# Optimization experiments

Measured on AMD Instinct MI355X. Metric: run time of the kernel, lower is better.

The kernel has to match this reference:

```python
import jax, jax.numpy as jnp
import numpy as np

B, S, H, NH, L, FF, V, T = 16, 256, 768, 12, 12, 3072, 30522, 9
DH = H // NH
LN_EPS = 1e-12


def _ln(x, g, b):
    m = jnp.mean(x, axis=-1, keepdims=True)
    v = jnp.mean((x - m) ** 2, axis=-1, keepdims=True)
    return (x - m) * jax.lax.rsqrt(v + LN_EPS) * g + b


def setup_inputs():
    key = jax.random.key(0)
    ks = jax.random.split(key, 20)
    n = lambda i, shape: jax.random.normal(ks[i], shape, jnp.float32) * 0.02
    lengths = jax.random.randint(ks[0], (B,), S // 2, S + 1)
    attention_mask = (jnp.arange(S)[None, :] < lengths[:, None]).astype(jnp.int32)
    return {
        "input_ids": jax.random.randint(ks[1], (B, S), 0, V),
        "attention_mask": attention_mask,
        "labels": jax.random.randint(ks[2], (B, S), 0, T),
        "word_emb": n(3, (V, H)),
        "pos_emb": n(4, (512, H)),
        "type_emb": n(5, (2, H)),
        "emb_g": jnp.ones((H,), jnp.float32), "emb_b": jnp.zeros((H,), jnp.float32),
        "lWq": n(6, (L, H, H)), "lbq": jnp.zeros((L, H), jnp.float32),
        "lWk": n(7, (L, H, H)), "lbk": jnp.zeros((L, H), jnp.float32),
        "lWv": n(8, (L, H, H)), "lbv": jnp.zeros((L, H), jnp.float32),
        "lWo": n(9, (L, H, H)), "lbo": jnp.zeros((L, H), jnp.float32),
        "lg1": jnp.ones((L, H), jnp.float32), "lb1": jnp.zeros((L, H), jnp.float32),
        "lWi": n(10, (L, H, FF)), "lbi": jnp.zeros((L, FF), jnp.float32),
        "lWf": n(11, (L, FF, H)), "lbf": jnp.zeros((L, H), jnp.float32),
        "lg2": jnp.ones((L, H), jnp.float32), "lb2": jnp.zeros((L, H), jnp.float32),
        "cls_W": n(12, (H, T)), "cls_b": jnp.zeros((T,), jnp.float32),
        "crf_start": jax.random.uniform(ks[13], (T,), jnp.float32, -0.1, 0.1),
        "crf_end": jax.random.uniform(ks[14], (T,), jnp.float32, -0.1, 0.1),
        "crf_trans": jax.random.uniform(ks[15], (T, T), jnp.float32, -0.1, 0.1),
    }


def _encoder(input_ids, attention_mask, word_emb, pos_emb, type_emb, emb_g, emb_b, layer_stack, cls_W, cls_b):
    x = word_emb[input_ids] + pos_emb[:S][None] + type_emb[0][None, None]  # [B,S,H]
    x = _ln(x, emb_g, emb_b)
    bias = (1.0 - attention_mask.astype(jnp.float32))[:, None, None, :] * -1e9  # [B,1,1,S]
    scale = 1.0 / np.sqrt(DH).astype(np.float32)

    def layer(h, p):
        Wq, bq, Wk, bk, Wv, bv, Wo, bo, g1, b1, Wi, bi, Wf, bf, g2, b2 = p
        q = (h @ Wq + bq).reshape(B, S, NH, DH)
        k = (h @ Wk + bk).reshape(B, S, NH, DH)
        v = (h @ Wv + bv).reshape(B, S, NH, DH)
        att = jax.nn.softmax(jnp.einsum('bqhd,bkhd->bhqk', q, k) * scale + bias, axis=-1)
        ctx = jnp.einsum('bhqk,bkhd->bqhd', att, v).reshape(B, S, H)
        h = _ln(h + ctx @ Wo + bo, g1, b1)
        ff = jax.nn.gelu(h @ Wi + bi, approximate=False) @ Wf + bf
        h = _ln(h + ff, g2, b2)
        return h, None

    x, _ = jax.lax.scan(layer, x, layer_stack)
    return x @ cls_W + cls_b  # [B,S,T]


def _crf_llh(em, tg, m, start, end, trans):
    # pytorch-crf forward, reduction='sum'. em [B,Lc,T], tg [B,Lc] int, m [B,Lc] bool
    mf = m.astype(em.dtype)
    em_sc = jnp.take_along_axis(em, tg[..., None], axis=-1)[..., 0]  # [B,Lc]
    tr_sc = trans[tg[:, :-1], tg[:, 1:]]                             # [B,Lc-1]
    num = start[tg[:, 0]] + em_sc[:, 0] + jnp.sum(mf[:, 1:] * (tr_sc + em_sc[:, 1:]), axis=1)
    seq_ends = jnp.sum(m.astype(jnp.int32), axis=1) - 1
    last_tag = jnp.take_along_axis(tg, seq_ends[:, None], axis=1)[:, 0]
    num = num + end[last_tag]

    def step(score, xs):
        em_t, m_t = xs
        nxt = jax.nn.logsumexp(score[:, :, None] + trans[None] + em_t[:, None, :], axis=1)
        return jnp.where(m_t[:, None], nxt, score), None

    score0 = start[None] + em[:, 0]
    score, _ = jax.lax.scan(step, score0, (em[:, 1:].transpose(1, 0, 2), m[:, 1:].transpose(1, 0)))
    den = jax.nn.logsumexp(score + end[None], axis=1)
    return jnp.sum(num - den)


def _viterbi(em, start, end, trans):
    # decode over the FULL sequence with all-ones mask (matches crf.decode(logits))
    def step(score, em_t):
        cand = score[:, :, None] + trans[None] + em_t[:, None, :]  # [B,T,T]
        return jnp.max(cand, axis=1), jnp.argmax(cand, axis=1)

    score0 = start[None] + em[:, 0]
    score, hist = jax.lax.scan(step, score0, em[:, 1:].transpose(1, 0, 2))  # hist [S-1,B,T]
    last = jnp.argmax(score + end[None], axis=1)  # [B]

    def back(tag, h):
        prev = jnp.take_along_axis(h, tag[:, None], axis=1)[:, 0]
        return prev, prev

    _, rev = jax.lax.scan(back, last, hist, reverse=True)  # rev[i] = tag at time i, i in [0,S-2]
    tags = jnp.concatenate([rev.transpose(1, 0), last[:, None]], axis=1)  # [B,S]
    return tags.astype(jnp.float32)


def reference(input_ids, attention_mask, labels, word_emb, pos_emb, type_emb, emb_g, emb_b,
              lWq, lbq, lWk, lbk, lWv, lbv, lWo, lbo, lg1, lb1, lWi, lbi, lWf, lbf, lg2, lb2,
              cls_W, cls_b, crf_start, crf_end, crf_trans):
    layer_stack = (lWq, lbq, lWk, lbk, lWv, lbv, lWo, lbo, lg1, lb1, lWi, lbi, lWf, lbf, lg2, lb2)
    logits = _encoder(input_ids, attention_mask, word_emb, pos_emb, type_emb, emb_g, emb_b, layer_stack, cls_W, cls_b)
    str_lens = jnp.sum(attention_mask, axis=-1)
    pos = jnp.arange(S)[None, :]
    mask = attention_mask.astype(bool) & (pos > 0) & (pos != (str_lens - 1)[:, None])
    tags_in = jnp.where(mask, labels, jnp.zeros_like(labels))
    loss = -_crf_llh(logits[:, 1:], tags_in[:, 1:], mask[:, 1:], crf_start, crf_end, crf_trans)
    tags = _viterbi(logits, crf_start, crf_end, crf_trans)
    return (loss, tags)
```

## Files before the change

kernel.cpp:

```cpp
#include <hip/hip_runtime.h>

#define B_ 16
#define S_ 256
#define H_ 768
#define NH_ 12
#define DH_ 64
#define L_ 12
#define FF_ 3072
#define T_ 9
#define NTOK (B_*S_)

#define AS1 __attribute__((address_space(1)))
#define AS3 __attribute__((address_space(3)))

typedef __attribute__((ext_vector_type(8))) short bfrag;
typedef __attribute__((ext_vector_type(8))) unsigned short us8;
typedef __attribute__((ext_vector_type(4))) float f4;

#define LOG2E_ 1.4426950408889634f
#define LN2_   0.6931471805599453f

__device__ inline unsigned short f2bf(float x) {
    unsigned u = __builtin_bit_cast(unsigned, x);
    return (unsigned short)((u + 0x7fffu + ((u >> 16) & 1u)) >> 16);
}
__device__ inline float bf2f(unsigned short h) {
    unsigned u = ((unsigned)h) << 16;
    return __builtin_bit_cast(float, u);
}
__device__ inline void pack8(const float* v, us8& h, us8& l) {
    #pragma unroll
    for (int j = 0; j < 8; j++) {
        unsigned short hh = f2bf(v[j]);
        h[j] = hh;
        l[j] = f2bf(v[j] - bf2f(hh));
    }
}

__global__ __launch_bounds__(256) void k_conv_w(
    const float* __restrict__ Wq, const float* __restrict__ Wk,
    const float* __restrict__ Wv, const float* __restrict__ Wo,
    const float* __restrict__ Wi, const float* __restrict__ Wf,
    const float* __restrict__ bq, const float* __restrict__ bk, const float* __restrict__ bv,
    float* __restrict__ qkvbias, unsigned short* __restrict__ Wpk)
{
    int bid = blockIdx.x;
    int tid = threadIdx.x;
    if (bid == 0) {
        for (int i = tid; i < 3 * H_; i += 256)
            qkvbias[i] = (i < H_) ? bq[i] : (i < 2 * H_) ? bk[i - H_] : bv[i - 2 * H_];
    }
    const float* src; int Kd, Nd; size_t doff; int t;
    if (bid < 576)       { int m = bid / 144; src = (m == 0) ? Wq : (m == 1) ? Wk : (m == 2) ? Wv : Wo;
                           Kd = H_; Nd = H_; doff = (size_t)m * 73728; t = bid % 144; }
    else if (bid < 1152) { src = Wi; Kd = H_; Nd = FF_; doff = 294912; t = bid - 576; }
    else                 { src = Wf; Kd = FF_; Nd = H_; doff = 589824; t = bid - 1152; }
    int ntn = Nd / 64;
    int tk = t / ntn, tn = t % ntn;
    int k0 = tk * 64, n0 = tn * 64;
    __shared__ float tile[64][65];
    int r = tid >> 6, c = tid & 63;
    #pragma unroll
    for (int i = 0; i < 16; i++)
        tile[r + i * 4][c] = src[(size_t)(k0 + r + i * 4) * Nd + n0 + c];
    __syncthreads();
    #pragma unroll
    for (int e = 0; e < 2; e++) {
        int item = tid * 2 + e;
        int nl = item >> 3, kb = item & 7;
        float v8[8];
        #pragma unroll
        for (int j = 0; j < 8; j++) v8[j] = tile[kb * 8 + j][nl];
        us8 h, l; pack8(v8, h, l);
        unsigned short* p = Wpk + (doff + (size_t)(n0 + nl) * (Kd / 8) + (k0 / 8 + kb)) * 16;
        *reinterpret_cast<us8*>(p) = h;
        *reinterpret_cast<us8*>(p + 8) = l;
    }
}

__global__ __launch_bounds__(128) void k_embed_ln(
    const int* __restrict__ ids, const float* __restrict__ wemb,
    const float* __restrict__ pemb, const float* __restrict__ temb,
    const float* __restrict__ g, const float* __restrict__ bb,
    float* __restrict__ out, unsigned short* __restrict__ out_pk)
{
    int tok = blockIdx.x;
    int s = tok & (S_ - 1);
    int id = ids[tok];
    int tid = threadIdx.x;
    bool act = tid < 96;
    int idx = tid * 8;
    float v8[8];
    float sum = 0.f;
    if (act) {
        const float4* w4 = reinterpret_cast<const float4*>(wemb + (size_t)id * H_ + idx);
        const float4* p4 = reinterpret_cast<const float4*>(pemb + (size_t)s * H_ + idx);
        const float4* t4 = reinterpret_cast<const float4*>(temb + idx);
        #pragma unroll
        for (int q = 0; q < 2; q++) {
            float4 a = w4[q], b = p4[q], c = t4[q];
            v8[q*4+0] = a.x + b.x + c.x; v8[q*4+1] = a.y + b.y + c.y;
            v8[q*4+2] = a.z + b.z + c.z; v8[q*4+3] = a.w + b.w + c.w;
        }
        #pragma unroll
        for (int j = 0; j < 8; j++) sum += v8[j];
    }
    __shared__ float wsum[2], wvar[2];
    #pragma unroll
    for (int o = 32; o > 0; o >>= 1) sum += __shfl_xor(sum, o);
    if ((tid & 63) == 0) wsum[tid >> 6] = sum;
    __syncthreads();
    float mean = (wsum[0] + wsum[1]) * (1.0f / H_);
    float vs = 0.f;
    if (act) {
        for (int j = 0; j < 8; j++) { float d = v8[j] - mean; vs += d * d; }
    }
    #pragma unroll
    for (int o = 32; o > 0; o >>= 1) vs += __shfl_xor(vs, o);
    if ((tid & 63) == 0) wvar[tid >> 6] = vs;
    __syncthreads();
    float inv = 1.0f / sqrtf((wvar[0] + wvar[1]) * (1.0f / H_) + 1e-12f);
    if (act) {
        float o8[8];
        #pragma unroll
        for (int j = 0; j < 8; j++) o8[j] = (v8[j] - mean) * inv * g[idx + j] + bb[idx + j];
        float4* d4 = reinterpret_cast<float4*>(out + (size_t)tok * H_ + idx);
        d4[0] = make_float4(o8[0], o8[1], o8[2], o8[3]);
        d4[1] = make_float4(o8[4], o8[5], o8[6], o8[7]);
        us8 h, l; pack8(o8, h, l);
        unsigned short* p = out_pk + ((size_t)tok * 96 + tid) * 16;
        *reinterpret_cast<us8*>(p) = h;
        *reinterpret_cast<us8*>(p + 8) = l;
    }
}

__global__ __launch_bounds__(128) void k_res_ln(
    const float* __restrict__ x, const float* __restrict__ res,
    const float* __restrict__ g, const float* __restrict__ bb,
    float* __restrict__ out, unsigned short* __restrict__ out_pk)
{
    int tok = blockIdx.x;
    int tid = threadIdx.x;
    bool act = tid < 96;
    int idx = tid * 8;
    float v8[8];
    float sum = 0.f;
    if (act) {
        const float4* x4 = reinterpret_cast<const float4*>(x + (size_t)tok * H_ + idx);
        const float4* r4 = reinterpret_cast<const float4*>(res + (size_t)tok * H_ + idx);
        #pragma unroll
        for (int q = 0; q < 2; q++) {
            float4 a = x4[q], b = r4[q];
            v8[q*4+0] = a.x + b.x; v8[q*4+1] = a.y + b.y;
            v8[q*4+2] = a.z + b.z; v8[q*4+3] = a.w + b.w;
        }
        #pragma unroll
        for (int j = 0; j < 8; j++) sum += v8[j];
    }
    __shared__ float wsum[2], wvar[2];
    #pragma unroll
    for (int o = 32; o > 0; o >>= 1) sum += __shfl_xor(sum, o);
    if ((tid & 63) == 0) wsum[tid >> 6] = sum;
    __syncthreads();
    float mean = (wsum[0] + wsum[1]) * (1.0f / H_);
    float vs = 0.f;
    if (act) {
        for (int j = 0; j < 8; j++) { float d = v8[j] - mean; vs += d * d; }
    }
    #pragma unroll
    for (int o = 32; o > 0; o >>= 1) vs += __shfl_xor(vs, o);
    if ((tid & 63) == 0) wvar[tid >> 6] = vs;
    __syncthreads();
    float inv = 1.0f / sqrtf((wvar[0] + wvar[1]) * (1.0f / H_) + 1e-12f);
    if (act) {
        float o8[8];
        #pragma unroll
        for (int j = 0; j < 8; j++) o8[j] = (v8[j] - mean) * inv * g[idx + j] + bb[idx + j];
        float4* d4 = reinterpret_cast<float4*>(out + (size_t)tok * H_ + idx);
        d4[0] = make_float4(o8[0], o8[1], o8[2], o8[3]);
        d4[1] = make_float4(o8[4], o8[5], o8[6], o8[7]);
        us8 h, l; pack8(o8, h, l);
        unsigned short* p = out_pk + ((size_t)tok * 96 + tid) * 16;
        *reinterpret_cast<us8*>(p) = h;
        *reinterpret_cast<us8*>(p + 8) = l;
    }
}

template<int WNF>
__global__ __launch_bounds__(256) void k_gemm_pk(
    const unsigned short* __restrict__ A, const unsigned short* __restrict__ Wp,
    const float* __restrict__ bias,
    float* __restrict__ C0, float* __restrict__ C1, float* __restrict__ C2, int cpb,
    unsigned short* __restrict__ Cpk,
    int M, int N, int K, int act)
{
    constexpr int BN = WNF * 32;
    constexpr int BUFSZ = 16384 + BN * 128;
    __shared__ char smem[2 * BUFSZ];
    unsigned smb = (unsigned)(size_t)(void*)smem;

    int nbx = N / BN;
    int nwg = (M >> 7) * nbx;
    int id = blockIdx.x;
    int cpx = nwg >> 3;
    int swz = (id & 7) * cpx + (id >> 3);
    int by = swz / nbx, bx = swz % nbx;
    int m0 = by << 7, n0 = bx * BN;
    int Kb = K >> 3;
    int nst = Kb >> 2;
    int rowbytes = Kb * 32;

    int tid = threadIdx.x;
    int lane = tid & 63, wid = tid >> 6;
    int wm = wid >> 1, wn = wid & 1;
    int fr = lane & 15, fq = lane >> 4;

    f4 acc[4][WNF];
    #pragma unroll
    for (int i = 0; i < 4; i++)
        #pragma unroll
        for (int j = 0; j < WNF; j++) acc[i][j] = (f4){0.f, 0.f, 0.f, 0.f};

    const char* agp[4];
    const char* bgp[WNF];
    #pragma unroll
    for (int i = 0; i < 4; i++) {
        int d = i * 4096 + tid * 16;
        int row = d >> 7;
        int colp = (d & 127) ^ ((row & 7) << 4);
        agp[i] = (const char*)A + (size_t)(m0 + row) * rowbytes + colp;
    }
    #pragma unroll
    for (int i = 0; i < WNF; i++) {
        int d = i * 4096 + tid * 16;
        int row = d >> 7;
        int colp = (d & 127) ^ ((row & 7) << 4);
        bgp[i] = (const char*)Wp + (size_t)(n0 + row) * rowbytes + colp;
    }

    int afo[4], bfo[WNF];
    #pragma unroll
    for (int mi = 0; mi < 4; mi++) {
        int r = wm * 64 + mi * 16 + fr;
        afo[mi] = r * 128 + ((fq * 32) ^ ((r & 7) << 4));
    }
    #pragma unroll
    for (int ni = 0; ni < WNF; ni++) {
        int rb = wn * (WNF * 16) + ni * 16 + fr;
        bfo[ni] = rb * 128 + ((fq * 32) ^ ((rb & 7) << 4));
    }

    #pragma unroll
    for (int i = 0; i < 4; i++)
        __builtin_amdgcn_global_load_lds((const AS1 void*)(size_t)agp[i],
            (AS3 void*)(unsigned)(smb + i * 4096 + wid * 1024), 16, 0, 0);
    #pragma unroll
    for (int i = 0; i < WNF; i++)
        __builtin_amdgcn_global_load_lds((const AS1 void*)(size_t)bgp[i],
            (AS3 void*)(unsigned)(smb + 16384 + i * 4096 + wid * 1024), 16, 0, 0);
    asm volatile("s_waitcnt vmcnt(0)" ::: "memory");
    __builtin_amdgcn_s_barrier();
    __builtin_amdgcn_sched_barrier(0);

    for (int ks = 0; ks < nst; ks++) {
        unsigned cb = (unsigned)(ks & 1) * BUFSZ;
        unsigned nb2 = BUFSZ - cb;
        if (ks + 1 < nst) {
            size_t ko = (size_t)(ks + 1) * 128;
            #pragma unroll
            for (int i = 0; i < 4; i++)
                __builtin_amdgcn_global_load_lds((const AS1 void*)(size_t)(agp[i] + ko),
                    (AS3 void*)(unsigned)(smb + nb2 + i * 4096 + wid * 1024), 16, 0, 0);
            #pragma unroll
            for (int i = 0; i < WNF; i++)
                __builtin_amdgcn_global_load_lds((const AS1 void*)(size_t)(bgp[i] + ko),
                    (AS3 void*)(unsigned)(smb + nb2 + 16384 + i * 4096 + wid * 1024), 16, 0, 0);
        }
        const char* cbp = smem + cb;
        bfrag ah[4], al[4], bh[WNF], bl[WNF];
        #pragma unroll
        for (int mi = 0; mi < 4; mi++) {
            ah[mi] = *reinterpret_cast<const bfrag*>(cbp + afo[mi]);
            al[mi] = *reinterpret_cast<const bfrag*>(cbp + (afo[mi] ^ 16));
        }
        #pragma unroll
        for (int ni = 0; ni < WNF; ni++) {
            bh[ni] = *reinterpret_cast<const bfrag*>(cbp + 16384 + bfo[ni]);
            bl[ni] = *reinterpret_cast<const bfrag*>(cbp + 16384 + (bfo[ni] ^ 16));
        }
        #pragma unroll
        for (int mi = 0; mi < 4; mi++) {
            #pragma unroll
            for (int ni = 0; ni < WNF; ni++) {
                acc[mi][ni] = __builtin_amdgcn_mfma_f32_16x16x32_bf16(ah[mi], bh[ni], acc[mi][ni], 0, 0, 0);
                acc[mi][ni] = __builtin_amdgcn_mfma_f32_16x16x32_bf16(ah[mi], bl[ni], acc[mi][ni], 0, 0, 0);
                acc[mi][ni] = __builtin_amdgcn_mfma_f32_16x16x32_bf16(al[mi], bh[ni], acc[mi][ni], 0, 0, 0);
            }
        }
        asm volatile("s_waitcnt vmcnt(0)" ::: "memory");
        __builtin_amdgcn_s_barrier();
        __builtin_amdgcn_sched_barrier(0);
    }

    if (act == 0) {
        #pragma unroll
        for (int mi = 0; mi < 4; mi++) {
            #pragma unroll
            for (int ni = 0; ni < WNF; ni++) {
                int col = n0 + wn * (WNF * 16) + ni * 16 + fr;
                float bv = bias[col];
                int buf = col / cpb;
                float* Cp = (buf == 0) ? C0 : (buf == 1) ? C1 : C2;
                int cc = col - buf * cpb;
                #pragma unroll
                for (int r = 0; r < 4; r++) {
                    int row = m0 + wm * 64 + mi * 16 + fq * 4 + r;
                    Cp[(size_t)row * cpb + cc] = acc[mi][ni][r] + bv;
                }
            }
        }
    } else {
        float* ebuf = (float*)smem;
        int Nb = N >> 3;
        #pragma unroll
        for (int mi = 0; mi < 4; mi++) {
            #pragma unroll
            for (int ni = 0; ni < WNF; ni++) {
                int col = n0 + wn * (WNF * 16) + ni * 16 + fr;
                float bv = bias[col];
                #pragma unroll
                for (int r = 0; r < 4; r++) {
                    float v = acc[mi][ni][r] + bv;
                    v = 0.5f * v * (1.0f + erff(v * 0.70710678118654752f));
                    ebuf[(wid * 16 + fq * 4 + r) * 68 + ni * 16 + fr] = v;
                }
            }
            #pragma unroll
            for (int e = 0; e < 2; e++) {
                int item = lane * 2 + e;
                int row16 = item >> 3, kb = item & 7;
                float v8[8];
                #pragma unroll
                for (int j = 0; j < 8; j++) v8[j] = ebuf[(wid * 16 + row16) * 68 + kb * 8 + j];
                us8 h, l; pack8(v8, h, l);
                int grow = m0 + wm * 64 + mi * 16 + row16;
                int gcb = ((n0 + wn * 64) >> 3) + kb;
                unsigned short* p = Cpk + ((size_t)grow * Nb + gcb) * 16;
                *reinterpret_cast<us8*>(p) = h;
                *reinterpret_cast<us8*>(p + 8) = l;
            }
        }
    }
}

#define SM_KH 0
#define SM_KL 5632
#define SM_VH 11264
#define SM_VL 16384
#define SM_PH 21504
#define SM_PL 26624
__global__ __launch_bounds__(256) void k_attn_fused(
    const float* __restrict__ Q, const float* __restrict__ Kb,
    const float* __restrict__ V, const int* __restrict__ amask,
    unsigned short* __restrict__ ctx_pk)
{
    __shared__ char smem[31744];
    unsigned short* KhS = (unsigned short*)(smem + SM_KH);
    unsigned short* KlS = (unsigned short*)(smem + SM_KL);
    unsigned short* VhS = (unsigned short*)(smem + SM_VH);
    unsigned short* VlS = (unsigned short*)(smem + SM_VL);
    unsigned short* PhS = (unsigned short*)(smem + SM_PH);
    unsigned short* PlS = (unsigned short*)(smem + SM_PL);

    int idx = blockIdx.x;
    int qt = idx & 3;
    int hd = (idx >> 2) % NH_;
    int b = idx / (4 * NH_);
    int tid = threadIdx.x;
    int lane = tid & 63, wid = tid >> 6;
    int fr = lane & 15, fq = lane >> 4;

    int q0 = qt * 64 + wid * 16;

    bfrag qh[2], ql[2];
    {
        const float* qbase = Q + ((size_t)(b * S_ + q0 + fr)) * H_ + hd * DH_;
        #pragma unroll
        for (int ks = 0; ks < 2; ks++) {
            const float4* p = reinterpret_cast<const float4*>(qbase + ks * 32 + fq * 8);
            float4 v0 = p[0], v1 = p[1];
            float vv[8] = {v0.x, v0.y, v0.z, v0.w, v1.x, v1.y, v1.z, v1.w};
            #pragma unroll
            for (int j = 0; j < 8; j++) {
                unsigned short h = f2bf(vv[j]);
                qh[ks][j] = (short)h;
                ql[ks][j] = (short)f2bf(vv[j] - bf2f(h));
            }
        }
    }

    f4 o[4];
    #pragma unroll
    for (int i = 0; i < 4; i++) o[i] = (f4){0.f, 0.f, 0.f, 0.f};
    float m[4], l[4];
    #pragma unroll
    for (int r = 0; r < 4; r++) { m[r] = -3e38f; l[r] = 0.f; }

    int kvrow = tid >> 3;
    int dbase = (tid & 7) * 8;

    for (int t = 0; t < 8; t++) {
        {
            const float* src = Kb + ((size_t)(b * S_ + t * 32 + kvrow)) * H_ + hd * DH_ + dbase;
            float4 a4 = reinterpret_cast<const float4*>(src)[0];
            float4 b4 = reinterpret_cast<const float4*>(src)[1];
            float vv[8] = {a4.x, a4.y, a4.z, a4.w, b4.x, b4.y, b4.z, b4.w};
            us8 h, l2;
            #pragma unroll
            for (int j = 0; j < 8; j++) {
                unsigned short hh = f2bf(vv[j]);
                h[j] = hh; l2[j] = f2bf(vv[j] - bf2f(hh));
            }
            *reinterpret_cast<us8*>(&KhS[kvrow * 88 + dbase]) = h;
            *reinterpret_cast<us8*>(&KlS[kvrow * 88 + dbase]) = l2;
        }
        {
            const float* src = V + ((size_t)(b * S_ + t * 32 + kvrow)) * H_ + hd * DH_ + dbase;
            float4 a4 = reinterpret_cast<const float4*>(src)[0];
            float4 b4 = reinterpret_cast<const float4*>(src)[1];
            float vv[8] = {a4.x, a4.y, a4.z, a4.w, b4.x, b4.y, b4.z, b4.w};
            #pragma unroll
            for (int j = 0; j < 8; j++) {
                unsigned short h = f2bf(vv[j]);
                VhS[(dbase + j) * 40 + kvrow] = h;
                VlS[(dbase + j) * 40 + kvrow] = f2bf(vv[j] - bf2f(h));
            }
        }
        __syncthreads();

        f4 s0 = (f4){0.f,0.f,0.f,0.f}, s1 = (f4){0.f,0.f,0.f,0.f};
        #pragma unroll
        for (int ks = 0; ks < 2; ks++) {
            bfrag kbh0 = *reinterpret_cast<const bfrag*>(&KhS[fr * 88 + ks * 32 + fq * 8]);
            bfrag kbl0 = *reinterpret_cast<const bfrag*>(&KlS[fr * 88 + ks * 32 + fq * 8]);
            bfrag kbh1 = *reinterpret_cast<const bfrag*>(&KhS[(16 + fr) * 88 + ks * 32 + fq * 8]);
            bfrag kbl1 = *reinterpret_cast<const bfrag*>(&KlS[(16 + fr) * 88 + ks * 32 + fq * 8]);
            s0 = __builtin_amdgcn_mfma_f32_16x16x32_bf16(qh[ks], kbh0, s0, 0, 0, 0);
            s0 = __builtin_amdgcn_mfma_f32_16x16x32_bf16(qh[ks], kbl0, s0, 0, 0, 0);
            s0 = __builtin_amdgcn_mfma_f32_16x16x32_bf16(ql[ks], kbh0, s0, 0, 0, 0);
            s1 = __builtin_amdgcn_mfma_f32_16x16x32_bf16(qh[ks], kbh1, s1, 0, 0, 0);
            s1 = __builtin_amdgcn_mfma_f32_16x16x32_bf16(qh[ks], kbl1, s1, 0, 0, 0);
            s1 = __builtin_amdgcn_mfma_f32_16x16x32_bf16(ql[ks], kbh1, s1, 0, 0, 0);
        }

        float cb0 = (amask[b * S_ + t * 32 + fr] == 0) ? -1e9f : 0.f;
        float cb1 = (amask[b * S_ + t * 32 + 16 + fr] == 0) ? -1e9f : 0.f;
        float sc0[4], sc1[4], fct[4], pr0[4], pr1[4];
        #pragma unroll
        for (int r = 0; r < 4; r++) {
            sc0[r] = s0[r] * 0.125f + cb0;
            sc1[r] = s1[r] * 0.125f + cb1;
            float tm = fmaxf(sc0[r], sc1[r]);
            #pragma unroll
            for (int od = 1; od < 16; od <<= 1) tm = fmaxf(tm, __shfl_xor(tm, od));
            float mn = fmaxf(m[r], tm);
            fct[r] = expf(m[r] - mn);
            pr0[r] = expf(sc0[r] - mn);
            pr1[r] = expf(sc1[r] - mn);
            float rs = pr0[r] + pr1[r];
            #pragma unroll
            for (int od = 1; od < 16; od <<= 1) rs += __shfl_xor(rs, od);
            l[r] = l[r] * fct[r] + rs;
            m[r] = mn;
        }
        #pragma unroll
        for (int ci = 0; ci < 4; ci++)
            #pragma unroll
            for (int r = 0; r < 4; r++) o[ci][r] *= fct[r];

        #pragma unroll
        for (int r = 0; r < 4; r++) {
            int row = fq * 4 + r;
            unsigned short h0 = f2bf(pr0[r]);
            PhS[wid * 640 + row * 40 + fr] = h0;
            PlS[wid * 640 + row * 40 + fr] = f2bf(pr0[r] - bf2f(h0));
            unsigned short h1 = f2bf(pr1[r]);
            PhS[wid * 640 + row * 40 + 16 + fr] = h1;
            PlS[wid * 640 + row * 40 + 16 + fr] = f2bf(pr1[r] - bf2f(h1));
        }

        bfrag pah = *reinterpret_cast<const bfrag*>(&PhS[wid * 640 + fr * 40 + fq * 8]);
        bfrag pal = *reinterpret_cast<const bfrag*>(&PlS[wid * 640 + fr * 40 + fq * 8]);
        #pragma unroll
        for (int ci = 0; ci < 4; ci++) {
            bfrag vbh = *reinterpret_cast<const bfrag*>(&VhS[(ci * 16 + fr) * 40 + fq * 8]);
            bfrag vbl = *reinterpret_cast<const bfrag*>(&VlS[(ci * 16 + fr) * 40 + fq * 8]);
            o[ci] = __builtin_amdgcn_mfma_f32_16x16x32_bf16(pah, vbh, o[ci], 0, 0, 0);
            o[ci] = __builtin_amdgcn_mfma_f32_16x16x32_bf16(pah, vbl, o[ci], 0, 0, 0);
            o[ci] = __builtin_amdgcn_mfma_f32_16x16x32_bf16(pal, vbh, o[ci], 0, 0, 0);
        }
        __syncthreads();
    }

    __syncthreads();
    float* eb = (float*)smem + wid * 1088;
    #pragma unroll
    for (int r = 0; r < 4; r++) {
        float inv = 1.0f / l[r];
        #pragma unroll
        for (int ci = 0; ci < 4; ci++)
            eb[(fq * 4 + r) * 68 + ci * 16 + fr] = o[ci][r] * inv;
    }
    __syncthreads();
    #pragma unroll
    for (int e = 0; e < 2; e++) {
        int item = lane * 2 + e;
        int row16 = item >> 3, kb = item & 7;
        float v8[8];
        #pragma unroll
        for (int j = 0; j < 8; j++) v8[j] = eb[row16 * 68 + kb * 8 + j];
        us8 h, l2; pack8(v8, h, l2);
        int grow = b * S_ + q0 + row16;
        int gcb = hd * 8 + kb;
        unsigned short* p = ctx_pk + ((size_t)grow * 96 + gcb) * 16;
        *reinterpret_cast<us8*>(p) = h;
        *reinterpret_cast<us8*>(p + 8) = l2;
    }
}

__global__ __launch_bounds__(64) void k_classifier(
    const float* __restrict__ Hs, const float* __restrict__ Wc,
    const float* __restrict__ bc, float* __restrict__ logits)
{
    int tok = blockIdx.x;
    int lane = threadIdx.x;
    const float* hr = Hs + (size_t)tok * H_;
    float acc[T_];
    #pragma unroll
    for (int j = 0; j < T_; j++) acc[j] = 0.f;
    for (int k = lane; k < H_; k += 64) {
        float hv = hr[k];
        const float* wr = Wc + (size_t)k * T_;
        #pragma unroll
        for (int j = 0; j < T_; j++) acc[j] = fmaf(hv, wr[j], acc[j]);
    }
    #pragma unroll
    for (int j = 0; j < T_; j++) {
        float v = acc[j];
        for (int o = 32; o > 0; o >>= 1) v += __shfl_down(v, o);
        if (lane == 0) logits[(size_t)tok * T_ + j] = v + bc[j];
    }
}

__global__ __launch_bounds__(256) void k_crf_vit(
    const float* __restrict__ logits, const int* __restrict__ amask,
    const int* __restrict__ labels, const float* __restrict__ start,
    const float* __restrict__ endv, const float* __restrict__ trans,
    float* __restrict__ out)
{
    int blk = blockIdx.x;
    int tid = threadIdx.x;
    if (blk == 0) {
        __shared__ float res[B_];
        int lane = tid & 63;
        int bb = (tid >> 6) * 4 + (lane >> 4);
        int sj = lane & 15;
        int lb = lane & 48;

        int cnt = 0;
        for (int s = sj; s < S_; s += 16) cnt += amask[bb * S_ + s];
        #pragma unroll
        for (int o = 8; o > 0; o >>= 1) cnt += __shfl_xor(cnt, o);
        int len = cnt;
        int lim = len - 1;

        float num = 0.f;
        for (int s = 2 + sj; s < S_; s += 16) {
            if (s < lim) {
                int tp = labels[bb * S_ + s - 1];
                int tc = labels[bb * S_ + s];
                num += trans[tp * T_ + tc] + logits[((size_t)(bb * S_ + s)) * T_ + tc];
            }
        }
        #pragma unroll
        for (int o = 8; o > 0; o >>= 1) num += __shfl_xor(num, o);
        int tg1 = labels[bb * S_ + 1];
        num += start[tg1] + logits[((size_t)(bb * S_ + 1)) * T_ + tg1];
        num += endv[labels[bb * S_ + (len - 2)]];

        float tc9[T_];
        #pragma unroll
        for (int i = 0; i < T_; i++) tc9[i] = (sj < T_) ? trans[i * T_ + sj] * LOG2E_ : 0.f;
        float score = (sj < T_) ? (start[sj] + logits[((size_t)(bb * S_ + 1)) * T_ + sj]) * LOG2E_ : 0.f;
        const float* embase = logits + (size_t)bb * S_ * T_ + sj;
        float emb[8];
        #pragma unroll
        for (int c = 0; c < 8; c++) emb[c] = (sj < T_) ? embase[(2 + c) * T_] : 0.f;
        for (int s0 = 2; s0 < S_; s0 += 8) {
            #pragma unroll
            for (int c = 0; c < 8; c++) {
                int s = s0 + c;
                if (s < S_) {
                    float em = emb[c];
                    emb[c] = (sj < T_ && s + 8 < S_) ? embase[(size_t)(s + 8) * T_] : 0.f;
                    float si[T_];
                    #pragma unroll
                    for (int i = 0; i < T_; i++) si[i] = __shfl(score, lb + i);
                    float a9[T_];
                    #pragma unroll
                    for (int i = 0; i < T_; i++) a9[i] = si[i] + tc9[i];
                    float mx = a9[0];
                    #pragma unroll
                    for (int i = 1; i < T_; i++) mx = fmaxf(mx, a9[i]);
                    float sum = 0.f;
                    #pragma unroll
                    for (int i = 0; i < T_; i++) sum += exp2f(a9[i] - mx);
                    float nsc = fmaf(em, LOG2E_, mx + log2f(sum));
                    if (s < lim) score = nsc;
                }
            }
        }
        float se = (sj < T_) ? score + endv[sj] * LOG2E_ : -1e30f;
        float fi[T_];
        #pragma unroll
        for (int i = 0; i < T_; i++) fi[i] = __shfl(se, lb + i);
        if (sj == 0) {
            float mx = -1e30f;
            #pragma unroll
            for (int i = 0; i < T_; i++) mx = fmaxf(mx, fi[i]);
            float sum = 0.f;
            #pragma unroll
            for (int i = 0; i < T_; i++) sum += exp2f(fi[i] - mx);
            res[bb] = (mx + log2f(sum)) * LN2_ - num;
        }
        __syncthreads();
        if (tid == 0) {
            float tot = 0.f;
            #pragma unroll
            for (int i = 0; i < B_; i++) tot += res[i];
            out[0] = tot;
        }
    } else {
        if (tid >= 64) return;
        int b = blk - 1;
        int j = tid;
        float* tags_out = out + 1;
        __shared__ unsigned char hist[S_ - 1][T_];
        float tc9[T_];
        #pragma unroll
        for (int i = 0; i < T_; i++) tc9[i] = (j < T_) ? trans[i * T_ + j] : 0.f;
        float score = (j < T_) ? start[j] + logits[((size_t)(b * S_)) * T_ + j] : -1e30f;
        const float* embase = logits + (size_t)b * S_ * T_ + j;
        float emb[8];
        #pragma unroll
        for (int c = 0; c < 8; c++) emb[c] = (j < T_) ? embase[(1 + c) * T_] : 0.f;
        for (int t0 = 1; t0 < S_; t0 += 8) {
            #pragma unroll
            for (int c = 0; c < 8; c++) {
                int t = t0 + c;
                if (t < S_) {
                    float em = emb[c];
                    emb[c] = (j < T_ && t + 8 < S_) ? embase[(size_t)(t + 8) * T_] : 0.f;
                    float si[T_];
                    #pragma unroll
                    for (int i = 0; i < T_; i++) si[i] = __shfl(score, i);
                    float best = -1e30f; int bi = 0;
                    #pragma unroll
                    for (int i = 0; i < T_; i++) {
                        float cv = si[i] + tc9[i];
                        if (cv > best) { best = cv; bi = i; }
                    }
                    if (j < T_) {
                        hist[t - 1][j] = (unsigned char)bi;
                        score = best + em;
                    }
                }
            }
        }
        float se = (j < T_) ? score + endv[j] : -1e30f;
        float fi[T_];
        #pragma unroll
        for (int i = 0; i < T_; i++) fi[i] = __shfl(se, i);
        if (j == 0) {
            float best = -1e30f; int last = 0;
            #pragma unroll
            for (int i = 0; i < T_; i++) if (fi[i] > best) { best = fi[i]; last = i; }
            tags_out[b * S_ + (S_ - 1)] = (float)last;
            int cur = last;
            for (int t = S_ - 2; t >= 0; t--) {
                cur = hist[t][cur];
                tags_out[b * S_ + t] = (float)cur;
            }
        }
    }
}

extern "C" void kernel_launch(void* const* d_in, const int* in_sizes, int n_in,
                              void* d_out, int out_size, void* d_ws, size_t ws_size,
                              hipStream_t stream)
{
    const int*   input_ids = (const int*)d_in[0];
    const int*   amask     = (const int*)d_in[1];
    const int*   labels    = (const int*)d_in[2];
    const float* word_emb  = (const float*)d_in[3];
    const float* pos_emb   = (const float*)d_in[4];
    const float* type_emb  = (const float*)d_in[5];
    const float* emb_g     = (const float*)d_in[6];
    const float* emb_b     = (const float*)d_in[7];
    const float* lWq = (const float*)d_in[8];
    const float* lbq = (const float*)d_in[9];
    const float* lWk = (const float*)d_in[10];
    const float* lbk = (const float*)d_in[11];
    const float* lWv = (const float*)d_in[12];
    const float* lbv = (const float*)d_in[13];
    const float* lWo = (const float*)d_in[14];
    const float* lbo = (const float*)d_in[15];
    const float* lg1 = (const float*)d_in[16];
    const float* lb1 = (const float*)d_in[17];
    const float* lWi = (const float*)d_in[18];
    const float* lbi = (const float*)d_in[19];
    const float* lWf = (const float*)d_in[20];
    const float* lbf = (const float*)d_in[21];
    const float* lg2 = (const float*)d_in[22];
    const float* lb2 = (const float*)d_in[23];
    const float* cls_W = (const float*)d_in[24];
    const float* cls_b = (const float*)d_in[25];
    const float* crf_start = (const float*)d_in[26];
    const float* crf_end   = (const float*)d_in[27];
    const float* crf_trans = (const float*)d_in[28];

    float* out = (float*)d_out;
    float* ws = (float*)d_ws;

    const size_t NH32 = (size_t)NTOK * H_;
    float* h       = ws;
    float* h_pk_f  = ws + NH32;
    float* q       = ws + 2 * NH32;
    float* kbuf    = ws + 3 * NH32;
    float* v       = ws + 4 * NH32;
    float* ctxpk_f = ws + 5 * NH32;
    float* tmp     = ws + 6 * NH32;
    float* Wpk_f   = ws + 7 * NH32;
    float* qkvbias = Wpk_f + 7077888;
    float* logits  = qkvbias + 3 * H_;

    unsigned short* h_pk   = (unsigned short*)h_pk_f;
    unsigned short* ctx_pk = (unsigned short*)ctxpk_f;
    unsigned short* Wpk    = (unsigned short*)Wpk_f;
    unsigned short* big_pk = (unsigned short*)q;

    k_embed_ln<<<NTOK, 128, 0, stream>>>(input_ids, word_emb, pos_emb, type_emb, emb_g, emb_b, h, h_pk);

    const size_t WOFF_O = 221184, WOFF_I = 294912, WOFF_F = 589824;

    for (int l = 0; l < L_; l++) {
        k_conv_w<<<1728, 256, 0, stream>>>(
            lWq + (size_t)l * H_ * H_, lWk + (size_t)l * H_ * H_,
            lWv + (size_t)l * H_ * H_, lWo + (size_t)l * H_ * H_,
            lWi + (size_t)l * H_ * FF_, lWf + (size_t)l * FF_ * H_,
            lbq + (size_t)l * H_, lbk + (size_t)l * H_, lbv + (size_t)l * H_,
            qkvbias, Wpk);

        k_gemm_pk<4><<<576, 256, 0, stream>>>(h_pk, Wpk, qkvbias,
            q, kbuf, v, H_, nullptr, NTOK, 3 * H_, H_, 0);

        k_attn_fused<<<B_ * NH_ * 4, 256, 0, stream>>>(q, kbuf, v, amask, ctx_pk);

        k_gemm_pk<2><<<384, 256, 0, stream>>>(ctx_pk, Wpk + WOFF_O * 16, lbo + (size_t)l * H_,
            tmp, tmp, tmp, H_, nullptr, NTOK, H_, H_, 0);

        k_res_ln<<<NTOK, 128, 0, stream>>>(tmp, h, lg1 + (size_t)l * H_, lb1 + (size_t)l * H_, h, h_pk);

        k_gemm_pk<4><<<768, 256, 0, stream>>>(h_pk, Wpk + WOFF_I * 16, lbi + (size_t)l * FF_,
            tmp, tmp, tmp, FF_, big_pk, NTOK, FF_, H_, 1);

        k_gemm_pk<2><<<384, 256, 0, stream>>>(big_pk, Wpk + WOFF_F * 16, lbf + (size_t)l * H_,
            tmp, tmp, tmp, H_, nullptr, NTOK, H_, FF_, 0);

        k_res_ln<<<NTOK, 128, 0, stream>>>(tmp, h, lg2 + (size_t)l * H_, lb2 + (size_t)l * H_, h, h_pk);
    }

    k_classifier<<<NTOK, 64, 0, stream>>>(h, cls_W, cls_b, logits);
    k_crf_vit<<<1 + B_, 256, 0, stream>>>(logits, amask, labels, crf_start, crf_end, crf_trans, out);
}
```

Before: 3.598 ms.

## Triple-buffer GEMM loads, fix 128x64 tiles, and remap blocks per XCD

```diff
diff --git a/kernel.cpp b/kernel.cpp
--- a/kernel.cpp
+++ b/kernel.cpp
@@ -186,26 +186,23 @@
     }
 }
 
-template<int WNF>
 __global__ __launch_bounds__(256) void k_gemm_pk(
     const unsigned short* __restrict__ A, const unsigned short* __restrict__ Wp,
     const float* __restrict__ bias,
     float* __restrict__ C0, float* __restrict__ C1, float* __restrict__ C2, int cpb,
     unsigned short* __restrict__ Cpk,
-    int M, int N, int K, int act)
+    int M, int N, int K, int act, int cbx)
 {
-    constexpr int BN = WNF * 32;
-    constexpr int BUFSZ = 16384 + BN * 128;
-    __shared__ char smem[2 * BUFSZ];
+    constexpr int BUFSZ = 24576;
+    __shared__ char smem[3 * BUFSZ];
     unsigned smb = (unsigned)(size_t)(void*)smem;
 
-    int nbx = N / BN;
-    int nwg = (M >> 7) * nbx;
     int id = blockIdx.x;
-    int cpx = nwg >> 3;
-    int swz = (id & 7) * cpx + (id >> 3);
-    int by = swz / nbx, bx = swz % nbx;
-    int m0 = by << 7, n0 = bx * BN;
+    int xcd = id & 7;
+    int rr = id >> 3;
+    int by = (xcd >> 1) * 8 + rr / cbx;
+    int bx = (xcd & 1) * cbx + rr % cbx;
+    int m0 = by << 7, n0 = bx << 6;
     int Kb = K >> 3;
     int nst = Kb >> 2;
     int rowbytes = Kb * 32;
@@ -215,14 +212,14 @@
     int wm = wid >> 1, wn = wid & 1;
     int fr = lane & 15, fq = lane >> 4;
 
-    f4 acc[4][WNF];
+    f4 acc[4][2];
     #pragma unroll
     for (int i = 0; i < 4; i++)
         #pragma unroll
-        for (int j = 0; j < WNF; j++) acc[i][j] = (f4){0.f, 0.f, 0.f, 0.f};
+        for (int j = 0; j < 2; j++) acc[i][j] = (f4){0.f, 0.f, 0.f, 0.f};
 
     const char* agp[4];
-    const char* bgp[WNF];
+    const char* bgp[2];
     #pragma unroll
     for (int i = 0; i < 4; i++) {
         int d = i * 4096 + tid * 16;
@@ -231,83 +228,81 @@
         agp[i] = (const char*)A + (size_t)(m0 + row) * rowbytes + colp;
     }
     #pragma unroll
-    for (int i = 0; i < WNF; i++) {
+    for (int i = 0; i < 2; i++) {
         int d = i * 4096 + tid * 16;
         int row = d >> 7;
         int colp = (d & 127) ^ ((row & 7) << 4);
         bgp[i] = (const char*)Wp + (size_t)(n0 + row) * rowbytes + colp;
     }
 
-    int afo[4], bfo[WNF];
+    int afo[4], bfo[2];
     #pragma unroll
     for (int mi = 0; mi < 4; mi++) {
         int r = wm * 64 + mi * 16 + fr;
         afo[mi] = r * 128 + ((fq * 32) ^ ((r & 7) << 4));
     }
     #pragma unroll
-    for (int ni = 0; ni < WNF; ni++) {
-        int rb = wn * (WNF * 16) + ni * 16 + fr;
-        bfo[ni] = rb * 128 + ((fq * 32) ^ ((rb & 7) << 4));
-    }
-
-    #pragma unroll
-    for (int i = 0; i < 4; i++)
-        __builtin_amdgcn_global_load_lds((const AS1 void*)(size_t)agp[i],
-            (AS3 void*)(unsigned)(smb + i * 4096 + wid * 1024), 16, 0, 0);
-    #pragma unroll
-    for (int i = 0; i < WNF; i++)
-        __builtin_amdgcn_global_load_lds((const AS1 void*)(size_t)bgp[i],
-            (AS3 void*)(unsigned)(smb + 16384 + i * 4096 + wid * 1024), 16, 0, 0);
-    asm volatile("s_waitcnt vmcnt(0)" ::: "memory");
-    __builtin_amdgcn_s_barrier();
-    __builtin_amdgcn_sched_barrier(0);
+    for (int ni = 0; ni < 2; ni++) {
+        int rb = wn * 32 + ni * 16 + fr;
+        bfo[ni] = 16384 + rb * 128 + ((fq * 32) ^ ((rb & 7) << 4));
+    }
+
+    auto issue = [&](int ks, unsigned boff) {
+        size_t ko = (size_t)ks * 128;
+        #pragma unroll
+        for (int i = 0; i < 4; i++)
+            __builtin_amdgcn_global_load_lds((const AS1 void*)(size_t)(agp[i] + ko),
+                (AS3 void*)(unsigned)(smb + boff + i * 4096 + wid * 1024), 16, 0, 0);
+        #pragma unroll
+        for (int i = 0; i < 2; i++)
+            __builtin_amdgcn_global_load_lds((const AS1 void*)(size_t)(bgp[i] + ko),
+                (AS3 void*)(unsigned)(smb + boff + 16384 + i * 4096 + wid * 1024), 16, 0, 0);
+    };
+
+    issue(0, 0);
+    if (nst > 1) issue(1, BUFSZ);
+    unsigned c0 = 0, c1 = BUFSZ, c2 = 2 * BUFSZ;
 
     for (int ks = 0; ks < nst; ks++) {
-        unsigned cb = (unsigned)(ks & 1) * BUFSZ;
-        unsigned nb2 = BUFSZ - cb;
-        if (ks + 1 < nst) {
-            size_t ko = (size_t)(ks + 1) * 128;
-            #pragma unroll
-            for (int i = 0; i < 4; i++)
-                __builtin_amdgcn_global_load_lds((const AS1 void*)(size_t)(agp[i] + ko),
-                    (AS3 void*)(unsigned)(smb + nb2 + i * 4096 + wid * 1024), 16, 0, 0);
-            #pragma unroll
-            for (int i = 0; i < WNF; i++)
-                __builtin_amdgcn_global_load_lds((const AS1 void*)(size_t)(bgp[i] + ko),
-                    (AS3 void*)(unsigned)(smb + nb2 + 16384 + i * 4096 + wid * 1024), 16, 0, 0);
-        }
-        const char* cbp = smem + cb;
-        bfrag ah[4], al[4], bh[WNF], bl[WNF];
+        if (ks + 2 < nst) issue(ks + 2, c2);
+        if (ks + 2 < nst)      asm volatile("s_waitcnt vmcnt(12)" ::: "memory");
+        else if (ks + 1 < nst) asm volatile("s_waitcnt vmcnt(6)" ::: "memory");
+        else                   asm volatile("s_waitcnt vmcnt(0)" ::: "memory");
+        __builtin_amdgcn_s_barrier();
+        __builtin_amdgcn_sched_barrier(0);
+
+        const char* cbp = smem + c0;
+        bfrag ah[4], al[4], bh[2], bl[2];
         #pragma unroll
         for (int mi = 0; mi < 4; mi++) {
             ah[mi] = *reinterpret_cast<const bfrag*>(cbp + afo[mi]);
             al[mi] = *reinterpret_cast<const bfrag*>(cbp + (afo[mi] ^ 16));
         }
         #pragma unroll
-        for (int ni = 0; ni < WNF; ni++) {
-            bh[ni] = *reinterpret_cast<const bfrag*>(cbp + 16384 + bfo[ni]);
-            bl[ni] = *reinterpret_cast<const bfrag*>(cbp + 16384 + (bfo[ni] ^ 16));
+        for (int ni = 0; ni < 2; ni++) {
+            bh[ni] = *reinterpret_cast<const bfrag*>(cbp + bfo[ni]);
+            bl[ni] = *reinterpret_cast<const bfrag*>(cbp + (bfo[ni] ^ 16));
         }
         #pragma unroll
         for (int mi = 0; mi < 4; mi++) {
             #pragma unroll
-            for (int ni = 0; ni < WNF; ni++) {
+            for (int ni = 0; ni < 2; ni++) {
                 acc[mi][ni] = __builtin_amdgcn_mfma_f32_16x16x32_bf16(ah[mi], bh[ni], acc[mi][ni], 0, 0, 0);
                 acc[mi][ni] = __builtin_amdgcn_mfma_f32_16x16x32_bf16(ah[mi], bl[ni], acc[mi][ni], 0, 0, 0);
                 acc[mi][ni] = __builtin_amdgcn_mfma_f32_16x16x32_bf16(al[mi], bh[ni], acc[mi][ni], 0, 0, 0);
             }
         }
-        asm volatile("s_waitcnt vmcnt(0)" ::: "memory");
         __builtin_amdgcn_s_barrier();
         __builtin_amdgcn_sched_barrier(0);
+        unsigned t = c0; c0 = c1; c1 = c2; c2 = t;
     }
 
     if (act == 0) {
         #pragma unroll
         for (int mi = 0; mi < 4; mi++) {
             #pragma unroll
-            for (int ni = 0; ni < WNF; ni++) {
-                int col = n0 + wn * (WNF * 16) + ni * 16 + fr;
+            for (int ni = 0; ni < 2; ni++) {
+                int col = n0 + wn * 32 + ni * 16 + fr;
                 float bv = bias[col];
                 int buf = col / cpb;
                 float* Cp = (buf == 0) ? C0 : (buf == 1) ? C1 : C2;
@@ -320,35 +315,31 @@
             }
         }
     } else {
-        float* ebuf = (float*)smem;
+        float* ebuf = (float*)(smem + wid * 2432);
         int Nb = N >> 3;
         #pragma unroll
         for (int mi = 0; mi < 4; mi++) {
             #pragma unroll
-            for (int ni = 0; ni < WNF; ni++) {
-                int col = n0 + wn * (WNF * 16) + ni * 16 + fr;
+            for (int ni = 0; ni < 2; ni++) {
+                int col = n0 + wn * 32 + ni * 16 + fr;
                 float bv = bias[col];
                 #pragma unroll
                 for (int r = 0; r < 4; r++) {
                     float v = acc[mi][ni][r] + bv;
                     v = 0.5f * v * (1.0f + erff(v * 0.70710678118654752f));
-                    ebuf[(wid * 16 + fq * 4 + r) * 68 + ni * 16 + fr] = v;
+                    ebuf[(fq * 4 + r) * 38 + ni * 16 + fr] = v;
                 }
             }
-            #pragma unroll
-            for (int e = 0; e < 2; e++) {
-                int item = lane * 2 + e;
-                int row16 = item >> 3, kb = item & 7;
-                float v8[8];
-                #pragma unroll
-                for (int j = 0; j < 8; j++) v8[j] = ebuf[(wid * 16 + row16) * 68 + kb * 8 + j];
-                us8 h, l; pack8(v8, h, l);
-                int grow = m0 + wm * 64 + mi * 16 + row16;
-                int gcb = ((n0 + wn * 64) >> 3) + kb;
-                unsigned short* p = Cpk + ((size_t)grow * Nb + gcb) * 16;
-                *reinterpret_cast<us8*>(p) = h;
-                *reinterpret_cast<us8*>(p + 8) = l;
-            }
+            int row16 = lane >> 2, kb = lane & 3;
+            float v8[8];
+            #pragma unroll
+            for (int j = 0; j < 8; j++) v8[j] = ebuf[row16 * 38 + kb * 8 + j];
+            us8 h, l; pack8(v8, h, l);
+            int grow = m0 + wm * 64 + mi * 16 + row16;
+            int gcb = ((n0 + wn * 32) >> 3) + kb;
+            unsigned short* p = Cpk + ((size_t)grow * Nb + gcb) * 16;
+            *reinterpret_cast<us8*>(p) = h;
+            *reinterpret_cast<us8*>(p + 8) = l;
         }
     }
 }
@@ -761,21 +752,21 @@
             lbq + (size_t)l * H_, lbk + (size_t)l * H_, lbv + (size_t)l * H_,
             qkvbias, Wpk);
 
-        k_gemm_pk<4><<<576, 256, 0, stream>>>(h_pk, Wpk, qkvbias,
-            q, kbuf, v, H_, nullptr, NTOK, 3 * H_, H_, 0);
+        k_gemm_pk<<<1152, 256, 0, stream>>>(h_pk, Wpk, qkvbias,
+            q, kbuf, v, H_, nullptr, NTOK, 3 * H_, H_, 0, 18);
 
         k_attn_fused<<<B_ * NH_ * 4, 256, 0, stream>>>(q, kbuf, v, amask, ctx_pk);
 
-        k_gemm_pk<2><<<384, 256, 0, stream>>>(ctx_pk, Wpk + WOFF_O * 16, lbo + (size_t)l * H_,
-            tmp, tmp, tmp, H_, nullptr, NTOK, H_, H_, 0);
+        k_gemm_pk<<<384, 256, 0, stream>>>(ctx_pk, Wpk + WOFF_O * 16, lbo + (size_t)l * H_,
+            tmp, tmp, tmp, H_, nullptr, NTOK, H_, H_, 0, 6);
 
         k_res_ln<<<NTOK, 128, 0, stream>>>(tmp, h, lg1 + (size_t)l * H_, lb1 + (size_t)l * H_, h, h_pk);
 
-        k_gemm_pk<4><<<768, 256, 0, stream>>>(h_pk, Wpk + WOFF_I * 16, lbi + (size_t)l * FF_,
-            tmp, tmp, tmp, FF_, big_pk, NTOK, FF_, H_, 1);
-
-        k_gemm_pk<2><<<384, 256, 0, stream>>>(big_pk, Wpk + WOFF_F * 16, lbf + (size_t)l * H_,
-            tmp, tmp, tmp, H_, nullptr, NTOK, H_, FF_, 0);
+        k_gemm_pk<<<1536, 256, 0, stream>>>(h_pk, Wpk + WOFF_I * 16, lbi + (size_t)l * FF_,
+            tmp, tmp, tmp, FF_, big_pk, NTOK, FF_, H_, 1, 24);
+
+        k_gemm_pk<<<384, 256, 0, stream>>>(big_pk, Wpk + WOFF_F * 16, lbf + (size_t)l * H_,
+            tmp, tmp, tmp, H_, nullptr, NTOK, H_, FF_, 0, 6);
 
         k_res_ln<<<NTOK, 128, 0, stream>>>(tmp, h, lg2 + (size_t)l * H_, lb2 + (size_t)l * H_, h, h_pk);
     }
```

Result: no change. 3.608 ms (+0.3%).
